# Optimization experiments

Hardware: AMD Instinct MI355X
Metric: run time of the kernel (lower is better)

## Reference

```python
import jax, jax.numpy as jnp
import numpy as np

NEG_SLOPE_GAT = 0.2   # GATConv internal LeakyReLU
NEG_SLOPE_ACT = 0.01  # nn.LeakyReLU default
BN_EPS = 1e-5


def leaky(x, s):
    return jnp.where(x >= 0, x, s * x)


def gat_conv(x, src, dst, ea, W, We, a_s, a_d, a_e, b, n):
    # PyG GATConv, heads=1, concat=True, add_self_loops=True, fill_value='mean'.
    # src/dst already include appended self loops; ea includes mean-filled loop attrs.
    h = x @ W                      # [N, 64]
    e = ea @ We                    # [E+N, 64]
    alpha_src = h @ a_s            # [N]
    alpha_dst = h @ a_d            # [N]
    logits = leaky(alpha_src[src] + alpha_dst[dst] + e @ a_e, NEG_SLOPE_GAT)
    m = jax.ops.segment_max(logits, dst, num_segments=n)
    ex = jnp.exp(logits - m[dst])
    denom = jax.ops.segment_sum(ex, dst, num_segments=n)  # >0 (self loops)
    coef = ex / denom[dst]
    out = jax.ops.segment_sum(h[src] * coef[:, None], dst, num_segments=n)
    return out + b


def batch_norm(x, g, b):
    mu = x.mean(0)
    var = x.var(0)
    return (x - mu) / jnp.sqrt(var + BN_EPS) * g + b


def setup_inputs() -> dict:
    key = jax.random.key(0)
    N, E, H = 100000, 1600000, 64
    ks = jax.random.split(key, 40)
    d = {}
    d["x"] = jax.random.normal(ks[0], (N, 2), jnp.float32)
    d["edge_attr"] = jax.random.normal(ks[1], (E, 2), jnp.float32)
    d["edge_index"] = jax.random.randint(ks[2], (2, E), 0, N, jnp.int32)
    d["mask"] = jax.random.randint(ks[3], (N,), 0, 2, jnp.int32)
    i = 4
    for name, din in (("gcn", 2), ("lit", 2), ("gcn2", 64), ("lit2", 64)):
        d[name + "_W"] = jax.random.normal(ks[i], (din, H), jnp.float32) * 0.1; i += 1
        d[name + "_We"] = jax.random.normal(ks[i], (2, H), jnp.float32) * 0.1; i += 1
        d[name + "_as"] = jax.random.normal(ks[i], (H,), jnp.float32) * 0.1; i += 1
        d[name + "_ad"] = jax.random.normal(ks[i], (H,), jnp.float32) * 0.1; i += 1
        d[name + "_ae"] = jax.random.normal(ks[i], (H,), jnp.float32) * 0.1; i += 1
        d[name + "_b"] = jnp.zeros((H,), jnp.float32)
    d["ln_g"] = jnp.ones((H,), jnp.float32)
    d["ln_beta"] = jnp.zeros((H,), jnp.float32)
    d["f1_W"] = jax.random.normal(ks[i], (H, 32), jnp.float32) * 0.1; i += 1
    d["f1_b"] = jnp.zeros((32,), jnp.float32)
    d["f2_W"] = jax.random.normal(ks[i], (32, 1), jnp.float32) * 0.1
    d["f2_b"] = jnp.zeros((1,), jnp.float32)
    return d


def reference(x, edge_attr, edge_index, mask,
              gcn_W, gcn_We, gcn_as, gcn_ad, gcn_ae, gcn_b,
              lit_W, lit_We, lit_as, lit_ad, lit_ae, lit_b,
              gcn2_W, gcn2_We, gcn2_as, gcn2_ad, gcn2_ae, gcn2_b,
              lit2_W, lit2_We, lit2_as, lit2_ad, lit2_ae, lit2_b,
              ln_g, ln_beta, f1_W, f1_b, f2_W, f2_b):
    n = x.shape[0]
    loop = jnp.arange(n, dtype=edge_index.dtype)
    src = jnp.concatenate([edge_index[0], loop])
    dst = jnp.concatenate([edge_index[1], loop])
    ea = jnp.concatenate([edge_attr,
                          jnp.broadcast_to(edge_attr.mean(0), (n, edge_attr.shape[1]))], 0)
    mf = mask.astype(x.dtype)[:, None]  # [N,1]

    h = gat_conv(x, src, dst, ea, lit_W, lit_We, lit_as, lit_ad, lit_ae, lit_b, n) * (1 - mf) \
      + gat_conv(x, src, dst, ea, gcn_W, gcn_We, gcn_as, gcn_ad, gcn_ae, gcn_b, n) * mf
    h = leaky(batch_norm(h, ln_g, ln_beta), NEG_SLOPE_ACT)

    h = gat_conv(h, src, dst, ea, lit2_W, lit2_We, lit2_as, lit2_ad, lit2_ae, lit2_b, n) * (1 - mf) \
      + gat_conv(h, src, dst, ea, gcn2_W, gcn2_We, gcn2_as, gcn2_ad, gcn2_ae, gcn2_b, n) * mf
    h = leaky(h, NEG_SLOPE_ACT)

    out = (leaky(h @ f1_W + f1_b, NEG_SLOPE_ACT) @ f2_W + f2_b)[:, 0]
    return out * mask.astype(out.dtype)
```

## Files before the change

kernel.cpp:

```cpp
#include <hip/hip_runtime.h>

#define NEG_GAT 0.2f
#define NEG_ACT 0.01f
#define BN_EPS 1e-5f

__device__ __forceinline__ float wred64(float v) {
  #pragma unroll
  for (int o = 32; o; o >>= 1) v += __shfl_down(v, o);
  return v;
}
__device__ __forceinline__ int wredi64(int v) {
  #pragma unroll
  for (int o = 32; o; o >>= 1) v += __shfl_down(v, o);
  return v;
}
__device__ __forceinline__ int wscani(int x, int lane) {
  #pragma unroll
  for (int off = 1; off < 64; off <<= 1) {
    int t = __shfl_up(x, off);
    if (lane >= off) x += t;
  }
  return x;
}

__global__ void k_prep(const float* WL1, const float* WeL1, const float* asL1,
                       const float* adL1, const float* aeL1,
                       const float* WG1, const float* WeG1, const float* asG1,
                       const float* adG1, const float* aeG1,
                       const float* WL2, const float* WeL2, const float* asL2,
                       const float* adL2, const float* aeL2,
                       const float* WG2, const float* WeG2, const float* asG2,
                       const float* adG2, const float* aeG2,
                       float* ae2, float* l1c, float* was2) {
  int lane = threadIdx.x;
  const float* We[4] = {WeL1, WeG1, WeL2, WeG2};
  const float* ae[4] = {aeL1, aeG1, aeL2, aeG2};
  for (int s = 0; s < 4; s++) {
    float v0 = wred64(We[s][lane] * ae[s][lane]);
    float v1 = wred64(We[s][64 + lane] * ae[s][lane]);
    if (lane == 0) { ae2[2 * s] = v0; ae2[2 * s + 1] = v1; }
  }
  const float* W1[2] = {WL1, WG1};
  const float* a1s[2] = {asL1, asG1};
  const float* a1d[2] = {adL1, adG1};
  for (int t = 0; t < 2; t++) {
    float ws0 = wred64(W1[t][lane] * a1s[t][lane]);
    float ws1 = wred64(W1[t][64 + lane] * a1s[t][lane]);
    float wd0 = wred64(W1[t][lane] * a1d[t][lane]);
    float wd1 = wred64(W1[t][64 + lane] * a1d[t][lane]);
    if (lane == 0) {
      l1c[4 * t + 0] = ws0; l1c[4 * t + 1] = ws1;
      l1c[4 * t + 2] = wd0; l1c[4 * t + 3] = wd1;
    }
  }
  const float* W2[2] = {WL2, WG2};
  const float* a2s[2] = {asL2, asG2};
  const float* a2d[2] = {adL2, adG2};
  for (int t = 0; t < 2; t++) {
    float ss = 0.f, sd = 0.f;
    for (int j = 0; j < 64; j++) {
      float w = W2[t][lane * 64 + j];
      ss += w * a2s[t][j];
      sd += w * a2d[t][j];
    }
    was2[(2 * t) * 64 + lane] = ss;
    was2[(2 * t + 1) * 64 + lane] = sd;
  }
}

__global__ void __launch_bounds__(256)
k_eamean(const float* __restrict__ eattr, float* acc, int E) {
  int i = blockIdx.x * blockDim.x + threadIdx.x;
  float s0 = 0.f, s1 = 0.f;
  for (int e = i; e < E; e += gridDim.x * blockDim.x) {
    float2 v = ((const float2*)eattr)[e];
    s0 += v.x; s1 += v.y;
  }
  s0 = wred64(s0);
  s1 = wred64(s1);
  if ((threadIdx.x & 63) == 0) {
    atomicAdd(&acc[0], s0);
    atomicAdd(&acc[1], s1);
  }
}

__global__ void __launch_bounds__(256)
k_hist(const int* __restrict__ ei, int* __restrict__ cnt, int E) {
  int e = blockIdx.x * blockDim.x + threadIdx.x;
  if (e < E) atomicAdd(&cnt[ei[E + e]], 1);
}

__global__ void __launch_bounds__(256)
k_scanA(const int* __restrict__ cnt, int* __restrict__ bsum, int N) {
  __shared__ int wsum[4];
  int tid = threadIdx.x, lane = tid & 63, wid = tid >> 6;
  int base = blockIdx.x * 1024 + tid * 4;
  int t = 0;
  if (base + 3 < N) {
    int4 q = *(const int4*)(cnt + base);
    t = q.x + q.y + q.z + q.w;
  } else {
    if (base < N) t += cnt[base];
    if (base + 1 < N) t += cnt[base + 1];
    if (base + 2 < N) t += cnt[base + 2];
    if (base + 3 < N) t += cnt[base + 3];
  }
  t = wredi64(t);
  if (lane == 0) wsum[wid] = t;
  __syncthreads();
  if (tid == 0) bsum[blockIdx.x] = wsum[0] + wsum[1] + wsum[2] + wsum[3];
}

__global__ void __launch_bounds__(1024)
k_scanB(int* __restrict__ bsum, int* __restrict__ offs, int nb, int E, int N) {
  __shared__ int wsum[16];
  int tid = threadIdx.x, lane = tid & 63, wid = tid >> 6;
  int v = (tid < nb) ? bsum[tid] : 0;
  int x = wscani(v, lane);
  if (lane == 63) wsum[wid] = x;
  __syncthreads();
  if (wid == 0) {
    int w = (lane < 16) ? wsum[lane] : 0;
    w = wscani(w, lane);
    if (lane < 16) wsum[lane] = w;
  }
  __syncthreads();
  int incl = x + (wid ? wsum[wid - 1] : 0);
  if (tid < nb) bsum[tid] = incl - v;
  if (tid == 0) offs[N] = E;
}

__global__ void __launch_bounds__(256)
k_scanC(const int* __restrict__ cnt, const int* __restrict__ bsum,
        int* __restrict__ offs, int* __restrict__ cur, int N) {
  __shared__ int wsum[4];
  int tid = threadIdx.x, lane = tid & 63, wid = tid >> 6;
  int base = blockIdx.x * 1024 + tid * 4;
  int v0 = 0, v1 = 0, v2 = 0, v3 = 0;
  if (base + 3 < N) {
    int4 q = *(const int4*)(cnt + base);
    v0 = q.x; v1 = q.y; v2 = q.z; v3 = q.w;
  } else {
    if (base < N) v0 = cnt[base];
    if (base + 1 < N) v1 = cnt[base + 1];
    if (base + 2 < N) v2 = cnt[base + 2];
    if (base + 3 < N) v3 = cnt[base + 3];
  }
  int t = v0 + v1 + v2 + v3;
  int incl = wscani(t, lane);
  int exclT = incl - t;
  if (lane == 63) wsum[wid] = incl;
  __syncthreads();
  int wb = 0;
  if (wid > 0) wb += wsum[0];
  if (wid > 1) wb += wsum[1];
  if (wid > 2) wb += wsum[2];
  int eb = bsum[blockIdx.x] + wb + exclT;
  if (base < N)     { offs[base] = eb;           cur[base] = eb; }
  if (base + 1 < N) { int u = eb + v0;           offs[base + 1] = u; cur[base + 1] = u; }
  if (base + 2 < N) { int u = eb + v0 + v1;      offs[base + 2] = u; cur[base + 2] = u; }
  if (base + 3 < N) { int u = eb + v0 + v1 + v2; offs[base + 3] = u; cur[base + 3] = u; }
}

__global__ void __launch_bounds__(256)
k_node1(const float* __restrict__ x,
        const float* __restrict__ WL, const float* __restrict__ WG,
        const float* __restrict__ l1c,
        float* __restrict__ hL, float* __restrict__ hG,
        float* asL, float* adL, float* asG, float* adG, int N) {
  int idx = blockIdx.x * blockDim.x + threadIdx.x;
  int n = idx >> 6, lane = idx & 63;
  if (n >= N) return;
  float2 xv = ((const float2*)x)[n];
  hL[(size_t)n * 64 + lane] = xv.x * WL[lane] + xv.y * WL[64 + lane];
  hG[(size_t)n * 64 + lane] = xv.x * WG[lane] + xv.y * WG[64 + lane];
  if (lane == 0) {
    asL[n] = xv.x * l1c[0] + xv.y * l1c[1];
    adL[n] = xv.x * l1c[2] + xv.y * l1c[3];
    asG[n] = xv.x * l1c[4] + xv.y * l1c[5];
    adG[n] = xv.x * l1c[6] + xv.y * l1c[7];
  }
}

__global__ void __launch_bounds__(256)
k_fill(const int* __restrict__ ei, const float* __restrict__ eattr,
       const int* __restrict__ mask, const float* __restrict__ ae2,
       const float* __restrict__ asL1, const float* __restrict__ asG1,
       int* __restrict__ cur, int4* __restrict__ edg, int E) {
  int e = blockIdx.x * blockDim.x + threadIdx.x;
  if (e >= E) return;
  int s = ei[e], d = ei[E + e];
  int m = mask[d];
  float2 ea = ((const float2*)eattr)[e];
  float as1 = m ? asG1[s] : asL1[s];
  float t1 = as1 + ea.x * (m ? ae2[2] : ae2[0]) + ea.y * (m ? ae2[3] : ae2[1]);
  float t2 =       ea.x * (m ? ae2[6] : ae2[4]) + ea.y * (m ? ae2[7] : ae2[5]);
  int j = atomicAdd(&cur[d], 1);
  edg[j] = make_int4(s, __float_as_int(t1), __float_as_int(t2), m);
}

__global__ void __launch_bounds__(256)
k_refill(const float* __restrict__ asL2, const float* __restrict__ asG2,
         int4* __restrict__ edg, int E) {
  int j = blockIdx.x * blockDim.x + threadIdx.x;
  if (j >= E) return;
  int4 v = edg[j];
  float as2 = (v.w ? asG2 : asL2)[v.x];
  edg[j].y = __float_as_int(as2 + __int_as_float(v.z));
}

__device__ __forceinline__ float gat_row(
    int n, int lane, int m,
    const int* __restrict__ offs, const int4* __restrict__ edg,
    const float* __restrict__ hL, const float* __restrict__ hG,
    const float* __restrict__ asL, const float* __restrict__ adL,
    const float* __restrict__ asG, const float* __restrict__ adG,
    const float* __restrict__ ae2, const float* __restrict__ eacc, float invE) {
  const float* as_p = m ? asG : asL;
  const float* h_p  = m ? hG  : hL;
  float ad = (m ? adG : adL)[n];
  float k0 = m ? ae2[2] : ae2[0];
  float k1 = m ? ae2[3] : ae2[1];
  float lg = as_p[n] + ad + (eacc[0] * invE) * k0 + (eacc[1] * invE) * k1;
  lg = lg >= 0.f ? lg : NEG_GAT * lg;
  float ex = __expf(lg);
  float denom = ex;
  float acc = ex * h_p[(size_t)n * 64 + lane];
  int j = offs[n], end = offs[n + 1];
  for (; j + 4 <= end; j += 4) {
    int4 v0 = edg[j], v1 = edg[j + 1], v2 = edg[j + 2], v3 = edg[j + 3];
    float h0 = h_p[(size_t)v0.x * 64 + lane];
    float h1 = h_p[(size_t)v1.x * 64 + lane];
    float h2 = h_p[(size_t)v2.x * 64 + lane];
    float h3 = h_p[(size_t)v3.x * 64 + lane];
    float l0 = __int_as_float(v0.y) + ad;
    float l1 = __int_as_float(v1.y) + ad;
    float l2 = __int_as_float(v2.y) + ad;
    float l3 = __int_as_float(v3.y) + ad;
    l0 = l0 >= 0.f ? l0 : NEG_GAT * l0;
    l1 = l1 >= 0.f ? l1 : NEG_GAT * l1;
    l2 = l2 >= 0.f ? l2 : NEG_GAT * l2;
    l3 = l3 >= 0.f ? l3 : NEG_GAT * l3;
    float e0 = __expf(l0), e1 = __expf(l1), e2 = __expf(l2), e3 = __expf(l3);
    denom += (e0 + e1) + (e2 + e3);
    acc = fmaf(e0, h0, acc);
    acc = fmaf(e1, h1, acc);
    acc = fmaf(e2, h2, acc);
    acc = fmaf(e3, h3, acc);
  }
  for (; j < end; j++) {
    int4 v = edg[j];
    float hv = h_p[(size_t)v.x * 64 + lane];
    float l = __int_as_float(v.y) + ad;
    l = l >= 0.f ? l : NEG_GAT * l;
    float e = __expf(l);
    denom += e;
    acc = fmaf(e, hv, acc);
  }
  return acc / denom;
}

__global__ void __launch_bounds__(256)
k_gat1(const int* __restrict__ offs, const int4* __restrict__ edg,
       const int* __restrict__ mask,
       const float* __restrict__ hL, const float* __restrict__ hG,
       const float* __restrict__ asL, const float* __restrict__ adL,
       const float* __restrict__ asG, const float* __restrict__ adG,
       const float* __restrict__ ae2, const float* __restrict__ eacc,
       float invE, const float* __restrict__ bL,
       const float* __restrict__ bG, float* __restrict__ C, int N) {
  int idx = blockIdx.x * blockDim.x + threadIdx.x;
  int n = idx >> 6, lane = idx & 63;
  if (n >= N) return;
  int m = mask[n];
  float v = gat_row(n, lane, m, offs, edg, hL, hG,
                    asL, adL, asG, adG, ae2, eacc, invE);
  C[(size_t)n * 64 + lane] = v + (m ? bG[lane] : bL[lane]);
}

__global__ void __launch_bounds__(256)
k_bnstat(const float* __restrict__ C, float* sums, float* sq, int N) {
  __shared__ float ls[256], lq[256];
  int col = threadIdx.x & 63, rg = threadIdx.x >> 6;
  float s = 0.f, q = 0.f;
  for (int r = blockIdx.x * 4 + rg; r < N; r += gridDim.x * 4) {
    float v = C[(size_t)r * 64 + col];
    s += v; q += v * v;
  }
  ls[threadIdx.x] = s; lq[threadIdx.x] = q;
  __syncthreads();
  if (rg == 0) {
    s = ls[col] + ls[col + 64] + ls[col + 128] + ls[col + 192];
    q = lq[col] + lq[col + 64] + lq[col + 128] + lq[col + 192];
    atomicAdd(&sums[col], s);
    atomicAdd(&sq[col], q);
  }
}

__global__ void __launch_bounds__(256)
k_node2(const float* __restrict__ C,
        const float* __restrict__ sums, const float* __restrict__ sq,
        const float* __restrict__ g, const float* __restrict__ beta,
        const float* __restrict__ WL, const float* __restrict__ WG,
        const float* __restrict__ was2,
        float* __restrict__ hL, float* __restrict__ hG,
        float* asL, float* adL, float* asG, float* adG, int N) {
  int idx = blockIdx.x * blockDim.x + threadIdx.x;
  int n = idx >> 6, lane = idx & 63;
  if (n >= N) return;
  float invN = 1.0f / (float)N;
  float mu = sums[lane] * invN;
  float var = sq[lane] * invN - mu * mu;
  float v = C[(size_t)n * 64 + lane];
  v = (v - mu) * rsqrtf(var + BN_EPS) * g[lane] + beta[lane];
  float c = v >= 0.f ? v : NEG_ACT * v;
  float d0 = wred64(c * was2[lane]);
  float d1 = wred64(c * was2[64 + lane]);
  float d2 = wred64(c * was2[128 + lane]);
  float d3 = wred64(c * was2[192 + lane]);
  if (lane == 0) { asL[n] = d0; adL[n] = d1; asG[n] = d2; adG[n] = d3; }
  float accL = 0.f, accG = 0.f;
  #pragma unroll
  for (int k = 0; k < 64; k++) {
    float cb = __shfl(c, k);
    accL += cb * WL[k * 64 + lane];
    accG += cb * WG[k * 64 + lane];
  }
  hL[(size_t)n * 64 + lane] = accL;
  hG[(size_t)n * 64 + lane] = accG;
}

__global__ void __launch_bounds__(256)
k_gat2_mlp(const int* __restrict__ offs, const int4* __restrict__ edg,
           const int* __restrict__ mask,
           const float* __restrict__ hL, const float* __restrict__ hG,
           const float* __restrict__ asL, const float* __restrict__ adL,
           const float* __restrict__ asG, const float* __restrict__ adG,
           const float* __restrict__ ae2, const float* __restrict__ eacc,
           float invE, const float* __restrict__ bL,
           const float* __restrict__ bG,
           const float* __restrict__ f1W, const float* __restrict__ f1b,
           const float* __restrict__ f2W, const float* __restrict__ f2b,
           float* __restrict__ out, int N) {
  int idx = blockIdx.x * blockDim.x + threadIdx.x;
  int n = idx >> 6, lane = idx & 63;
  if (n >= N) return;
  int m = mask[n];
  float c = gat_row(n, lane, m, offs, edg, hL, hG,
                    asL, adL, asG, adG, ae2, eacc, invE)
          + (m ? bG[lane] : bL[lane]);
  c = c >= 0.f ? c : NEG_ACT * c;
  float acc = 0.f;
  #pragma unroll
  for (int k = 0; k < 64; k++) {
    float cb = __shfl(c, k);
    if (lane < 32) acc += cb * f1W[k * 32 + lane];
  }
  float p = 0.f;
  if (lane < 32) {
    float t = acc + f1b[lane];
    t = t >= 0.f ? t : NEG_ACT * t;
    p = t * f2W[lane];
  }
  p = wred64(p);
  if (lane == 0) out[n] = (p + f2b[0]) * (float)m;
}

extern "C" void kernel_launch(void* const* d_in, const int* in_sizes, int n_in,
                              void* d_out, int out_size, void* d_ws, size_t ws_size,
                              hipStream_t stream) {
  const float* x     = (const float*)d_in[0];
  const float* eattr = (const float*)d_in[1];
  const int*   ei    = (const int*)d_in[2];
  const int*   mask  = (const int*)d_in[3];
  const float* gcn_W  = (const float*)d_in[4];
  const float* gcn_We = (const float*)d_in[5];
  const float* gcn_as = (const float*)d_in[6];
  const float* gcn_ad = (const float*)d_in[7];
  const float* gcn_ae = (const float*)d_in[8];
  const float* gcn_b  = (const float*)d_in[9];
  const float* lit_W  = (const float*)d_in[10];
  const float* lit_We = (const float*)d_in[11];
  const float* lit_as = (const float*)d_in[12];
  const float* lit_ad = (const float*)d_in[13];
  const float* lit_ae = (const float*)d_in[14];
  const float* lit_b  = (const float*)d_in[15];
  const float* gcn2_W  = (const float*)d_in[16];
  const float* gcn2_We = (const float*)d_in[17];
  const float* gcn2_as = (const float*)d_in[18];
  const float* gcn2_ad = (const float*)d_in[19];
  const float* gcn2_ae = (const float*)d_in[20];
  const float* gcn2_b  = (const float*)d_in[21];
  const float* lit2_W  = (const float*)d_in[22];
  const float* lit2_We = (const float*)d_in[23];
  const float* lit2_as = (const float*)d_in[24];
  const float* lit2_ad = (const float*)d_in[25];
  const float* lit2_ae = (const float*)d_in[26];
  const float* lit2_b  = (const float*)d_in[27];
  const float* ln_g    = (const float*)d_in[28];
  const float* ln_beta = (const float*)d_in[29];
  const float* f1W = (const float*)d_in[30];
  const float* f1b = (const float*)d_in[31];
  const float* f2W = (const float*)d_in[32];
  const float* f2b = (const float*)d_in[33];

  const int N = in_sizes[3];
  const int E = in_sizes[1] / 2;
  const size_t N64 = (size_t)N * 64;

  int4*  edg   = (int4*)d_ws;
  float* C     = (float*)(edg + E);
  float* A     = C + N64;
  float* B     = A + N64;
  int*   cnt   = (int*)(B + N64);
  float* sums  = (float*)(cnt + N);
  float* sq    = sums + 64;
  float* eacc  = sq + 64;
  float* ae2   = eacc + 2;
  float* l1c   = ae2 + 8;
  float* was2  = l1c + 8;
  int*   offs  = (int*)(was2 + 256);
  int*   cur   = offs + N + 1;
  int*   bsum  = cur + N;
  float* asL   = (float*)(bsum + 1024);
  float* adL   = asL + N;
  float* asG   = adL + N;
  float* adG   = asG + N;

  const float invE = 1.0f / (float)E;
  const int TB = 256;
  const int nodeBlocks = (int)((N64 + TB - 1) / TB);
  const int eBlocks = (E + TB - 1) / TB;
  const int nb = (N + 1023) / 1024;

  hipMemsetAsync(cnt, 0, ((size_t)N + 130) * sizeof(float), stream);

  k_prep<<<1, 64, 0, stream>>>(lit_W, lit_We, lit_as, lit_ad, lit_ae,
                               gcn_W, gcn_We, gcn_as, gcn_ad, gcn_ae,
                               lit2_W, lit2_We, lit2_as, lit2_ad, lit2_ae,
                               gcn2_W, gcn2_We, gcn2_as, gcn2_ad, gcn2_ae,
                               ae2, l1c, was2);
  k_eamean<<<1024, TB, 0, stream>>>(eattr, eacc, E);
  k_hist<<<eBlocks, TB, 0, stream>>>(ei, cnt, E);
  k_scanA<<<nb, TB, 0, stream>>>(cnt, bsum, N);
  k_scanB<<<1, 1024, 0, stream>>>(bsum, offs, nb, E, N);
  k_scanC<<<nb, TB, 0, stream>>>(cnt, bsum, offs, cur, N);
  k_node1<<<nodeBlocks, TB, 0, stream>>>(x, lit_W, gcn_W, l1c,
                                         A, B, asL, adL, asG, adG, N);
  k_fill<<<eBlocks, TB, 0, stream>>>(ei, eattr, mask, ae2, asL, asG,
                                     cur, edg, E);
  k_gat1<<<nodeBlocks, TB, 0, stream>>>(offs, edg, mask, A, B,
                                        asL, adL, asG, adG, ae2, eacc, invE,
                                        lit_b, gcn_b, C, N);
  k_bnstat<<<384, TB, 0, stream>>>(C, sums, sq, N);
  k_node2<<<nodeBlocks, TB, 0, stream>>>(C, sums, sq, ln_g, ln_beta,
                                         lit2_W, gcn2_W, was2,
                                         A, B, asL, adL, asG, adG, N);
  k_refill<<<eBlocks, TB, 0, stream>>>(asL, asG, edg, E);
  k_gat2_mlp<<<nodeBlocks, TB, 0, stream>>>(offs, edg, mask, A, B,
                                            asL, adL, asG, adG, ae2 + 4, eacc, invE,
                                            lit2_b, gcn2_b, f1W, f1b, f2W, f2b,
                                            (float*)d_out, N);
}
```

Measured before the change: 881.6 us.

## Split wavefront into four edge groups with float4 neighbor feature gathers

The per-node GAT aggregation now splits each 64-lane wavefront into four 16-lane groups. Each group processes a different edge and loads a neighbor's 64-float feature row as float4s, with partial sums combined by xor shuffles at the end. This cuts the number of serial loop iterations per node and widens memory transactions, aiming to raise memory-level parallelism in the latency-bound gather. The cost is clamped, redundant loads for tail edges, extra shuffle reductions, and extra work in the MLP epilogue to redistribute the float4 results.

```diff
diff --git a/kernel.cpp b/kernel.cpp
--- a/kernel.cpp
+++ b/kernel.cpp
@@ -209,7 +209,7 @@
   edg[j].y = __float_as_int(as2 + __int_as_float(v.z));
 }
 
-__device__ __forceinline__ float gat_row(
+__device__ __forceinline__ float4 gat_row4(
     int n, int lane, int m,
     const int* __restrict__ offs, const int4* __restrict__ edg,
     const float* __restrict__ hL, const float* __restrict__ hG,
@@ -217,47 +217,47 @@
     const float* __restrict__ asG, const float* __restrict__ adG,
     const float* __restrict__ ae2, const float* __restrict__ eacc, float invE) {
   const float* as_p = m ? asG : asL;
-  const float* h_p  = m ? hG  : hL;
+  const float4* h4  = (const float4*)(m ? hG : hL);
   float ad = (m ? adG : adL)[n];
   float k0 = m ? ae2[2] : ae2[0];
   float k1 = m ? ae2[3] : ae2[1];
+  int sub = lane & 15, grp = lane >> 4;
   float lg = as_p[n] + ad + (eacc[0] * invE) * k0 + (eacc[1] * invE) * k1;
   lg = lg >= 0.f ? lg : NEG_GAT * lg;
-  float ex = __expf(lg);
-  float denom = ex;
-  float acc = ex * h_p[(size_t)n * 64 + lane];
+  float exs = __expf(lg);
+  float4 hs = h4[(size_t)n * 16 + sub];
+  float w = (grp == 0) ? exs : 0.f;
+  float ax = w * hs.x, ay = w * hs.y, az = w * hs.z, aw = w * hs.w;
+  float denom = w;
   int j = offs[n], end = offs[n + 1];
-  for (; j + 4 <= end; j += 4) {
-    int4 v0 = edg[j], v1 = edg[j + 1], v2 = edg[j + 2], v3 = edg[j + 3];
-    float h0 = h_p[(size_t)v0.x * 64 + lane];
-    float h1 = h_p[(size_t)v1.x * 64 + lane];
-    float h2 = h_p[(size_t)v2.x * 64 + lane];
-    float h3 = h_p[(size_t)v3.x * 64 + lane];
-    float l0 = __int_as_float(v0.y) + ad;
-    float l1 = __int_as_float(v1.y) + ad;
-    float l2 = __int_as_float(v2.y) + ad;
-    float l3 = __int_as_float(v3.y) + ad;
+  for (; j < end; j += 8) {
+    int i0 = j + grp, i1 = j + 4 + grp;
+    int c0 = i0 < end ? i0 : end - 1;
+    int c1 = i1 < end ? i1 : end - 1;
+    int4 r0 = edg[(size_t)c0];
+    int4 r1 = edg[(size_t)c1];
+    float4 h0 = h4[(size_t)r0.x * 16 + sub];
+    float4 h1 = h4[(size_t)r1.x * 16 + sub];
+    float l0 = __int_as_float(r0.y) + ad;
+    float l1 = __int_as_float(r1.y) + ad;
     l0 = l0 >= 0.f ? l0 : NEG_GAT * l0;
     l1 = l1 >= 0.f ? l1 : NEG_GAT * l1;
-    l2 = l2 >= 0.f ? l2 : NEG_GAT * l2;
-    l3 = l3 >= 0.f ? l3 : NEG_GAT * l3;
-    float e0 = __expf(l0), e1 = __expf(l1), e2 = __expf(l2), e3 = __expf(l3);
-    denom += (e0 + e1) + (e2 + e3);
-    acc = fmaf(e0, h0, acc);
-    acc = fmaf(e1, h1, acc);
-    acc = fmaf(e2, h2, acc);
-    acc = fmaf(e3, h3, acc);
-  }
-  for (; j < end; j++) {
-    int4 v = edg[j];
-    float hv = h_p[(size_t)v.x * 64 + lane];
-    float l = __int_as_float(v.y) + ad;
-    l = l >= 0.f ? l : NEG_GAT * l;
-    float e = __expf(l);
-    denom += e;
-    acc = fmaf(e, hv, acc);
-  }
-  return acc / denom;
+    float e0 = (i0 < end) ? __expf(l0) : 0.f;
+    float e1 = (i1 < end) ? __expf(l1) : 0.f;
+    denom += e0 + e1;
+    ax = fmaf(e0, h0.x, ax); ay = fmaf(e0, h0.y, ay);
+    az = fmaf(e0, h0.z, az); aw = fmaf(e0, h0.w, aw);
+    ax = fmaf(e1, h1.x, ax); ay = fmaf(e1, h1.y, ay);
+    az = fmaf(e1, h1.z, az); aw = fmaf(e1, h1.w, aw);
+  }
+  #pragma unroll
+  for (int off = 16; off < 64; off <<= 1) {
+    ax += __shfl_xor(ax, off); ay += __shfl_xor(ay, off);
+    az += __shfl_xor(az, off); aw += __shfl_xor(aw, off);
+    denom += __shfl_xor(denom, off);
+  }
+  float inv = 1.f / denom;
+  return make_float4(ax * inv, ay * inv, az * inv, aw * inv);
 }
 
 __global__ void __launch_bounds__(256)
@@ -273,9 +273,13 @@
   int n = idx >> 6, lane = idx & 63;
   if (n >= N) return;
   int m = mask[n];
-  float v = gat_row(n, lane, m, offs, edg, hL, hG,
-                    asL, adL, asG, adG, ae2, eacc, invE);
-  C[(size_t)n * 64 + lane] = v + (m ? bG[lane] : bL[lane]);
+  float4 o = gat_row4(n, lane, m, offs, edg, hL, hG,
+                      asL, adL, asG, adG, ae2, eacc, invE);
+  if (lane < 16) {
+    float4 b4 = ((const float4*)(m ? bG : bL))[lane];
+    o.x += b4.x; o.y += b4.y; o.z += b4.z; o.w += b4.w;
+    ((float4*)C)[(size_t)n * 16 + lane] = o;
+  }
 }
 
 __global__ void __launch_bounds__(256)
@@ -346,15 +350,20 @@
   int n = idx >> 6, lane = idx & 63;
   if (n >= N) return;
   int m = mask[n];
-  float c = gat_row(n, lane, m, offs, edg, hL, hG,
-                    asL, adL, asG, adG, ae2, eacc, invE)
-          + (m ? bG[lane] : bL[lane]);
-  c = c >= 0.f ? c : NEG_ACT * c;
+  float4 o = gat_row4(n, lane, m, offs, edg, hL, hG,
+                      asL, adL, asG, adG, ae2, eacc, invE);
+  float4 b4 = ((const float4*)(m ? bG : bL))[lane & 15];
+  float cv[4];
+  cv[0] = o.x + b4.x; cv[1] = o.y + b4.y;
+  cv[2] = o.z + b4.z; cv[3] = o.w + b4.w;
+  #pragma unroll
+  for (int q = 0; q < 4; q++)
+    cv[q] = cv[q] >= 0.f ? cv[q] : NEG_ACT * cv[q];
   float acc = 0.f;
   #pragma unroll
   for (int k = 0; k < 64; k++) {
-    float cb = __shfl(c, k);
-    if (lane < 32) acc += cb * f1W[k * 32 + lane];
+    float cb = __shfl(cv[k & 3], k >> 2);
+    if (lane < 32) acc = fmaf(cb, f1W[k * 32 + lane], acc);
   }
   float p = 0.f;
   if (lane < 32) {
```

After: 865.8 us. No clear change (-1.8%).
